# Kernel optimization log

Measured on AMD Instinct MI355X. Metric: run time of the kernel, lower is better.

## Reference

```python
import jax, jax.numpy as jnp
import numpy as np

HID = 2048      # hidden_size
EXP = 64        # moe_num_experts
TOPK = 2        # moe_top_k
TOL = 1e-4
EPS = 1e-8


def setup_inputs() -> dict:
    key = jax.random.key(0)
    kx, kw = jax.random.split(key)
    x = jax.random.normal(kx, (2048, 8, HID), dtype=jnp.float32)          # (sl, bs, hs)
    W = jax.random.normal(kw, (EXP, HID), dtype=jnp.float32) * 0.02       # router weight (E, H)
    return {"x": x, "W": W}


def sinkhorn(cost, tol=TOL):
    """Iterative Sinkhorn normalization of a (tokens, experts) cost matrix."""
    cost = jnp.exp(cost)
    n0, n1 = cost.shape

    def cond(state):
        _, _, err = state
        return err > tol

    def body(state):
        _, d1_old, _ = state
        d0 = (1.0 / n0) / (jnp.sum(d1_old * cost, axis=1) + EPS)           # (tokens,)
        d1 = (1.0 / n1) / (jnp.sum(d0[:, None] * cost, axis=0) + EPS)      # (experts,)
        err = jnp.mean(jnp.abs(d1_old - d1))
        return (d0, d1, err)

    d0 = jnp.ones((n0,), cost.dtype)
    d1 = jnp.ones((n1,), cost.dtype)
    err0 = jnp.asarray(1e9, cost.dtype)
    d0, d1, _ = jax.lax.while_loop(cond, body, (d0, d1, err0))
    return d1 * cost * d0[:, None]


def reference(x, W):
    # Training-mode path on expert-parallel rank 0 (single device reference).
    tokens = x.reshape(-1, x.shape[-1])                                    # (sl*bs, H)
    logits = tokens @ W.T                                                  # (sl*bs, E)
    # Sinkhorn assignment is computed under no_grad in the original.
    norm_logits = sinkhorn(jax.lax.stop_gradient(logits.astype(jnp.float32)))
    _, indices = jax.lax.top_k(norm_logits, TOPK)                          # (sl*bs, top_k)
    # top_k > 1 -> softmax activation (in fp32, cast back)
    probs = jax.nn.softmax(logits.astype(jnp.float32), axis=-1).astype(logits.dtype)
    scores = jnp.take_along_axis(probs, indices, axis=1)                   # (sl*bs, top_k)
    return scores, indices
```

## Files before the change

kernel.cpp:

```cpp
#include <hip/hip_runtime.h>
#include <hip/hip_cooperative_groups.h>
#include <math.h>

#define HID   2048
#define NEXP  64
#define NTOK  16384
#define SBLK  64
#define TOLF  1e-4f
#define EPSF  1e-8f

typedef _Float16 f16x8 __attribute__((ext_vector_type(8)));
typedef float    f32x4 __attribute__((ext_vector_type(4)));

__device__ __forceinline__ void cvt8(const float4 a, const float4 b,
                                     f16x8& h, f16x8& l) {
    const float v[8] = {a.x, a.y, a.z, a.w, b.x, b.y, b.z, b.w};
#pragma unroll
    for (int j = 0; j < 8; ++j) {
        const _Float16 hh = (_Float16)v[j];
        h[j] = hh;
        l[j] = (_Float16)((v[j] - (float)hh) * 2048.0f);
    }
}

#define BSTRIDE 40
#define BUFELTS (8 * 64 * BSTRIDE)

__global__ __launch_bounds__(1024, 4) void gemm_mfma(const float* __restrict__ x,
                                                     const float* __restrict__ W,
                                                     float* __restrict__ L,
                                                     int* __restrict__ cnt) {
    __shared__ __align__(16) char smem[81920];
    _Float16* Bs0 = (_Float16*)smem;
    _Float16* Bs1 = Bs0 + BUFELTS;
    float*    red = (float*)smem;

    const int tid    = (int)threadIdx.x;
    if (blockIdx.x == 0 && tid == 0) *cnt = 0;

    const int waveid = tid >> 6;
    const int wt     = waveid >> 2;
    const int wk     = waveid & 3;
    const int lane   = tid & 63;
    const int lo     = lane & 15;
    const int hi     = lane >> 4;
    const int t0     = (int)blockIdx.x * 64;
    const int kb     = wk * 512;

    const int gt    = wt * 64 + lane;
    const int srow  = gt >> 2;
    const int sfrag = gt & 3;
    const float* sgp = W + (size_t)srow * HID + kb + sfrag * 8;
    const int swh = ((wk * 2 + 0) * 64 + srow) * BSTRIDE + sfrag * 8;
    const int swl = ((wk * 2 + 1) * 64 + srow) * BSTRIDE + sfrag * 8;

    const float* xp = x + (size_t)(t0 + wt * 16 + lo) * HID + kb + hi * 8;

    f32x4 acc_hh[4], acc_hl[4];
#pragma unroll
    for (int n = 0; n < 4; ++n) {
        acc_hh[n] = f32x4{0.f, 0.f, 0.f, 0.f};
        acc_hl[n] = f32x4{0.f, 0.f, 0.f, 0.f};
    }

    {
        const float4 v0 = *(const float4*)(sgp);
        const float4 v1 = *(const float4*)(sgp + 4);
        const float4 v2 = *(const float4*)(sgp + 32);
        const float4 v3 = *(const float4*)(sgp + 36);
        f16x8 h, l;
        cvt8(v0, v1, h, l);
        *(f16x8*)&Bs0[swh] = h;
        *(f16x8*)&Bs0[swl] = l;
        cvt8(v2, v3, h, l);
        *(f16x8*)&Bs1[swh] = h;
        *(f16x8*)&Bs1[swl] = l;
    }

    float4 a0n = *(const float4*)(xp);
    float4 a1n = *(const float4*)(xp + 4);
    __syncthreads();

    float4 sv0, sv1;

#pragma unroll 2
    for (int c = 0; c < 16; ++c) {
        if (c + 2 < 16) {
            sv0 = *(const float4*)(sgp + (c + 2) * 32);
            sv1 = *(const float4*)(sgp + (c + 2) * 32 + 4);
        }

        const float4 a0 = a0n, a1 = a1n;
        const int ko = ((c + 1 < 16) ? (c + 1) : 15) * 32;
        a0n = *(const float4*)(xp + ko);
        a1n = *(const float4*)(xp + ko + 4);

        const _Float16* Bc = (c & 1) ? Bs1 : Bs0;
        f16x8 bh[4], bl[4];
#pragma unroll
        for (int n = 0; n < 4; ++n) {
            bh[n] = *(const f16x8*)&Bc[((wk * 2 + 0) * 64 + lo + n * 16) * BSTRIDE + hi * 8];
            bl[n] = *(const f16x8*)&Bc[((wk * 2 + 1) * 64 + lo + n * 16) * BSTRIDE + hi * 8];
        }

        f16x8 ah, al;
        const float av[8] = {a0.x, a0.y, a0.z, a0.w, a1.x, a1.y, a1.z, a1.w};
#pragma unroll
        for (int j = 0; j < 8; ++j) {
            const _Float16 hh = (_Float16)av[j];
            ah[j] = hh;
            al[j] = (_Float16)((av[j] - (float)hh) * 2048.0f);
        }

#pragma unroll
        for (int n = 0; n < 4; ++n)
            acc_hh[n] = __builtin_amdgcn_mfma_f32_16x16x32_f16(ah, bh[n], acc_hh[n], 0, 0, 0);
#pragma unroll
        for (int n = 0; n < 4; ++n)
            acc_hl[n] = __builtin_amdgcn_mfma_f32_16x16x32_f16(ah, bl[n], acc_hl[n], 0, 0, 0);
#pragma unroll
        for (int n = 0; n < 4; ++n)
            acc_hl[n] = __builtin_amdgcn_mfma_f32_16x16x32_f16(al, bh[n], acc_hl[n], 0, 0, 0);

        __syncthreads();

        if (c + 2 < 16) {
            _Float16* Bw = (c & 1) ? Bs1 : Bs0;
            f16x8 h, l;
            cvt8(sv0, sv1, h, l);
            *(f16x8*)&Bw[swh] = h;
            *(f16x8*)&Bw[swl] = l;
        }
    }

#pragma unroll
    for (int n = 0; n < 4; ++n)
#pragma unroll
        for (int r = 0; r < 4; ++r)
            red[waveid * 1024 + n * 256 + r * 64 + lane] =
                acc_hh[n][r] + acc_hl[n][r] * (1.0f / 2048.0f);
    __syncthreads();

    {
        const int o      = tid * 4;
        const int t_loc  = o >> 6;
        const int e      = o & 63;
        const int wt_src = t_loc >> 4;
        const int tl     = t_loc & 15;
        const int idx    = (e >> 4) * 256 + (tl & 3) * 64 + (tl >> 2) * 16 + (e & 15);
        float4 s = *(const float4*)&red[(wt_src * 4 + 0) * 1024 + idx];
#pragma unroll
        for (int q = 1; q < 4; ++q) {
            const float4 v = *(const float4*)&red[(wt_src * 4 + q) * 1024 + idx];
            s.x += v.x; s.y += v.y; s.z += v.z; s.w += v.w;
        }
        *(float4*)(L + (size_t)(t0 + t_loc) * NEXP + e) = s;
    }
}

__device__ __forceinline__ float wave_sum64(float v) {
    int x;
    float t;
    x = __builtin_bit_cast(int, v);
    t = __builtin_bit_cast(float, __builtin_amdgcn_update_dpp(0, x, 0x111, 0xf, 0xf, true)); v += t;
    x = __builtin_bit_cast(int, v);
    t = __builtin_bit_cast(float, __builtin_amdgcn_update_dpp(0, x, 0x112, 0xf, 0xf, true)); v += t;
    x = __builtin_bit_cast(int, v);
    t = __builtin_bit_cast(float, __builtin_amdgcn_update_dpp(0, x, 0x114, 0xf, 0xf, true)); v += t;
    x = __builtin_bit_cast(int, v);
    t = __builtin_bit_cast(float, __builtin_amdgcn_update_dpp(0, x, 0x118, 0xf, 0xf, true)); v += t;
    x = __builtin_bit_cast(int, v);
    t = __builtin_bit_cast(float, __builtin_amdgcn_update_dpp(0, x, 0x142, 0xa, 0xf, true)); v += t;
    x = __builtin_bit_cast(int, v);
    t = __builtin_bit_cast(float, __builtin_amdgcn_update_dpp(0, x, 0x143, 0xc, 0xf, true)); v += t;
    return __builtin_bit_cast(float, __builtin_amdgcn_readlane(__builtin_bit_cast(int, v), 63));
}

__device__ __forceinline__ void grid_barrier(int* cnt, int target) {
    __syncthreads();
    if (threadIdx.x == 0) {
        __hip_atomic_fetch_add(cnt, 1, __ATOMIC_RELEASE, __HIP_MEMORY_SCOPE_AGENT);
        int it = 0;
        for (;;) {
            int v = __hip_atomic_load(cnt, __ATOMIC_RELAXED, __HIP_MEMORY_SCOPE_AGENT);
            if (v >= target) break;
            if ((++it & 7) == 0) {
                v = __hip_atomic_load(cnt, __ATOMIC_ACQUIRE, __HIP_MEMORY_SCOPE_AGENT);
                if (v >= target) break;
            }
            __builtin_amdgcn_s_sleep(1);
        }
        (void)__hip_atomic_load(cnt, __ATOMIC_ACQUIRE, __HIP_MEMORY_SCOPE_AGENT);
    }
    __syncthreads();
}

__global__ __launch_bounds__(1024) void sinkhorn_router(const float* __restrict__ L,
                                                        float* __restrict__ colbuf,
                                                        int* __restrict__ cnt,
                                                        float* __restrict__ out,
                                                        int nh) {
    __shared__ float part[16][64];
    __shared__ float redq[64][17];
    __shared__ float d1s[64];
    __shared__ float err_s;

    const int b     = blockIdx.x;
    const int tid   = (int)threadIdx.x;
    const int w     = tid >> 6;
    const int lane  = tid & 63;
    const int tbase = b * 256 + w * 16;

    float logit[16], cost[16], dreg[16];
#pragma unroll
    for (int j = 0; j < 16; ++j) {
        const int t = tbase + j;
        float l = L[(size_t)t * NEXP + lane];
        for (int h = 1; h < nh; ++h)
            l += L[(size_t)h * NTOK * NEXP + (size_t)t * NEXP + lane];
        logit[j] = l;
        cost[j]  = expf(l);
        dreg[j]  = 0.0f;
    }

    float d1l   = 1.0f;
    float d1old = 1.0f;
    int   g     = 0;

    for (;;) {
        float colacc = 0.0f;
#pragma unroll
        for (int j = 0; j < 16; ++j) {
            const float s = wave_sum64(d1l * cost[j]);
            const float d0 = (1.0f / 16384.0f) / (s + EPSF);
            dreg[j] = d0;
            colacc = fmaf(d0, cost[j], colacc);
        }
        part[w][lane] = colacc;
        __syncthreads();

        float* cb = colbuf + (size_t)(g & 1) * (NEXP * SBLK);
        if (tid < 64) {
            float s = part[0][tid];
#pragma unroll
            for (int q = 1; q < 16; ++q) s += part[q][tid];
            cb[tid * SBLK + b] = s;
        }
        grid_barrier(cnt, 64 * (g + 1));

        {
            const int e = tid >> 4;
            const int q = tid & 15;
            const float4 v = *(const float4*)(cb + e * SBLK + q * 4);
            redq[e][q] = (v.x + v.y) + (v.z + v.w);
        }
        __syncthreads();

        if (tid < 64) {
            float tot = redq[tid][0];
#pragma unroll
            for (int q = 1; q < 16; ++q) tot += redq[tid][q];
            const float d1n = (1.0f / 64.0f) / (tot + EPSF);
            float diff = fabsf(d1old - d1n);
#pragma unroll
            for (int m = 32; m; m >>= 1) diff += __shfl_xor(diff, m, 64);
            d1s[tid] = d1n;
            d1old    = d1n;
            if (tid == 0) err_s = diff * (1.0f / 64.0f);
        }
        __syncthreads();
        d1l = d1s[lane];
        const float err = err_s;
        ++g;
        if (!(err > TOLF) || g >= 512) break;
    }

#pragma unroll 1
    for (int j = 0; j < 16; ++j) {
        const int t = tbase + j;
        const float v = (d1l * cost[j]) * dreg[j];

        float bv = v; int bi = lane;
#pragma unroll
        for (int m = 32; m; m >>= 1) {
            const float ov = __shfl_xor(bv, m, 64);
            const int   oi = __shfl_xor(bi, m, 64);
            if (ov > bv || (ov == bv && oi < bi)) { bv = ov; bi = oi; }
        }
        const int i1 = bi;

        const float v2 = (lane == i1) ? -INFINITY : v;
        float bv2 = v2; int bi2 = lane;
#pragma unroll
        for (int m = 32; m; m >>= 1) {
            const float ov = __shfl_xor(bv2, m, 64);
            const int   oi = __shfl_xor(bi2, m, 64);
            if (ov > bv2 || (ov == bv2 && oi < bi2)) { bv2 = ov; bi2 = oi; }
        }
        const int i2 = bi2;

        float mx = logit[j];
#pragma unroll
        for (int m = 32; m; m >>= 1) mx = fmaxf(mx, __shfl_xor(mx, m, 64));
        const float e = expf(logit[j] - mx);
        float se = e;
#pragma unroll
        for (int m = 32; m; m >>= 1) se += __shfl_xor(se, m, 64);

        const float p1 = __shfl(e, i1, 64) / se;
        const float p2 = __shfl(e, i2, 64) / se;

        if (lane == 0) {
            out[(size_t)t * 2 + 0] = p1;
            out[(size_t)t * 2 + 1] = p2;
            out[(size_t)NTOK * 2 + (size_t)t * 2 + 0] = (float)i1;
            out[(size_t)NTOK * 2 + (size_t)t * 2 + 1] = (float)i2;
        }
    }
}

extern "C" void kernel_launch(void* const* d_in, const int* in_sizes, int n_in,
                              void* d_out, int out_size, void* d_ws, size_t ws_size,
                              hipStream_t stream) {
    const float* x = (const float*)d_in[0];
    const float* W = (const float*)d_in[1];
    float* out = (float*)d_out;

    float* L      = (float*)d_ws;
    float* colbuf = L + (size_t)NTOK * NEXP;
    int*   cnt    = (int*)(colbuf + 2 * NEXP * SBLK);

    gemm_mfma<<<dim3(256), dim3(1024), 0, stream>>>(x, W, L, cnt);

    int nh = 1;
    void* args[] = { (void*)&L, (void*)&colbuf, (void*)&cnt, (void*)&out, (void*)&nh };
    hipLaunchCooperativeKernel((void*)sinkhorn_router, dim3(SBLK), dim3(1024),
                               args, 0, stream);
}
```

Baseline: 274.8 us.

## Use hierarchical tree grid barrier and deepen GEMM prefetch pipeline

The flat single-counter grid barrier in the Sinkhorn kernel becomes a two-level tree: 8 padded leaf counters, a root counter and a generation flag that waiters poll. This spreads atomic contention across several cache lines. Separately, the GEMM loop now prefetches x two chunks ahead and W three chunks ahead, issuing those loads after the compute to hide global latency. The cost is more live registers, and the counter buffer must hold 320 ints, all zeroed by the first GEMM block.

```diff
diff --git a/kernel.cpp b/kernel.cpp
--- a/kernel.cpp
+++ b/kernel.cpp
@@ -25,6 +25,7 @@
 
 #define BSTRIDE 40
 #define BUFELTS (8 * 64 * BSTRIDE)
+#define LEAFSTRIDE 32
 
 __global__ __launch_bounds__(1024, 4) void gemm_mfma(const float* __restrict__ x,
                                                      const float* __restrict__ W,
@@ -35,8 +36,8 @@
     _Float16* Bs1 = Bs0 + BUFELTS;
     float*    red = (float*)smem;
 
-    const int tid    = (int)threadIdx.x;
-    if (blockIdx.x == 0 && tid == 0) *cnt = 0;
+    const int tid = (int)threadIdx.x;
+    if (blockIdx.x == 0 && tid < 10 * LEAFSTRIDE) cnt[tid] = 0;
 
     const int waveid = tid >> 6;
     const int wt     = waveid >> 2;
@@ -63,38 +64,29 @@
         acc_hl[n] = f32x4{0.f, 0.f, 0.f, 0.f};
     }
 
+    float4 sv0 = *(const float4*)(sgp);
+    float4 sv1 = *(const float4*)(sgp + 4);
     {
-        const float4 v0 = *(const float4*)(sgp);
-        const float4 v1 = *(const float4*)(sgp + 4);
-        const float4 v2 = *(const float4*)(sgp + 32);
-        const float4 v3 = *(const float4*)(sgp + 36);
+        const float4 t2 = *(const float4*)(sgp + 32);
+        const float4 t3 = *(const float4*)(sgp + 36);
         f16x8 h, l;
-        cvt8(v0, v1, h, l);
+        cvt8(sv0, sv1, h, l);
         *(f16x8*)&Bs0[swh] = h;
         *(f16x8*)&Bs0[swl] = l;
-        cvt8(v2, v3, h, l);
+        cvt8(t2, t3, h, l);
         *(f16x8*)&Bs1[swh] = h;
         *(f16x8*)&Bs1[swl] = l;
     }
-
-    float4 a0n = *(const float4*)(xp);
-    float4 a1n = *(const float4*)(xp + 4);
+    float4 a0c = *(const float4*)(xp);
+    float4 a1c = *(const float4*)(xp + 4);
+    float4 a0n = *(const float4*)(xp + 32);
+    float4 a1n = *(const float4*)(xp + 36);
+    sv0 = *(const float4*)(sgp + 64);
+    sv1 = *(const float4*)(sgp + 68);
     __syncthreads();
-
-    float4 sv0, sv1;
 
 #pragma unroll 2
     for (int c = 0; c < 16; ++c) {
-        if (c + 2 < 16) {
-            sv0 = *(const float4*)(sgp + (c + 2) * 32);
-            sv1 = *(const float4*)(sgp + (c + 2) * 32 + 4);
-        }
-
-        const float4 a0 = a0n, a1 = a1n;
-        const int ko = ((c + 1 < 16) ? (c + 1) : 15) * 32;
-        a0n = *(const float4*)(xp + ko);
-        a1n = *(const float4*)(xp + ko + 4);
-
         const _Float16* Bc = (c & 1) ? Bs1 : Bs0;
         f16x8 bh[4], bl[4];
 #pragma unroll
@@ -104,7 +96,7 @@
         }
 
         f16x8 ah, al;
-        const float av[8] = {a0.x, a0.y, a0.z, a0.w, a1.x, a1.y, a1.z, a1.w};
+        const float av[8] = {a0c.x, a0c.y, a0c.z, a0c.w, a1c.x, a1c.y, a1c.z, a1c.w};
 #pragma unroll
         for (int j = 0; j < 8; ++j) {
             const _Float16 hh = (_Float16)av[j];
@@ -130,6 +122,15 @@
             cvt8(sv0, sv1, h, l);
             *(f16x8*)&Bw[swh] = h;
             *(f16x8*)&Bw[swl] = l;
+        }
+        a0c = a0n; a1c = a1n;
+        if (c + 2 < 16) {
+            a0n = *(const float4*)(xp + (c + 2) * 32);
+            a1n = *(const float4*)(xp + (c + 2) * 32 + 4);
+        }
+        if (c + 3 < 16) {
+            sv0 = *(const float4*)(sgp + (c + 3) * 32);
+            sv1 = *(const float4*)(sgp + (c + 3) * 32 + 4);
         }
     }
 
@@ -176,21 +177,29 @@
     return __builtin_bit_cast(float, __builtin_amdgcn_readlane(__builtin_bit_cast(int, v), 63));
 }
 
-__device__ __forceinline__ void grid_barrier(int* cnt, int target) {
+__device__ __forceinline__ void grid_barrier(int* cnt, int g) {
     __syncthreads();
     if (threadIdx.x == 0) {
-        __hip_atomic_fetch_add(cnt, 1, __ATOMIC_RELEASE, __HIP_MEMORY_SCOPE_AGENT);
+        int* leaf = cnt + ((int)blockIdx.x & 7) * LEAFSTRIDE;
+        int* root = cnt + 8 * LEAFSTRIDE;
+        int* gen  = cnt + 9 * LEAFSTRIDE;
+        const int old = __hip_atomic_fetch_add(leaf, 1, __ATOMIC_ACQ_REL, __HIP_MEMORY_SCOPE_AGENT);
+        if ((old & 7) == 7) {
+            const int r = __hip_atomic_fetch_add(root, 1, __ATOMIC_ACQ_REL, __HIP_MEMORY_SCOPE_AGENT);
+            if ((r & 7) == 7)
+                __hip_atomic_store(gen, g + 1, __ATOMIC_RELEASE, __HIP_MEMORY_SCOPE_AGENT);
+        }
         int it = 0;
         for (;;) {
-            int v = __hip_atomic_load(cnt, __ATOMIC_RELAXED, __HIP_MEMORY_SCOPE_AGENT);
-            if (v >= target) break;
+            int v = __hip_atomic_load(gen, __ATOMIC_RELAXED, __HIP_MEMORY_SCOPE_AGENT);
+            if (v >= g + 1) break;
             if ((++it & 7) == 0) {
-                v = __hip_atomic_load(cnt, __ATOMIC_ACQUIRE, __HIP_MEMORY_SCOPE_AGENT);
-                if (v >= target) break;
+                v = __hip_atomic_load(gen, __ATOMIC_ACQUIRE, __HIP_MEMORY_SCOPE_AGENT);
+                if (v >= g + 1) break;
             }
             __builtin_amdgcn_s_sleep(1);
         }
-        (void)__hip_atomic_load(cnt, __ATOMIC_ACQUIRE, __HIP_MEMORY_SCOPE_AGENT);
+        (void)__hip_atomic_load(gen, __ATOMIC_ACQUIRE, __HIP_MEMORY_SCOPE_AGENT);
     }
     __syncthreads();
 }
@@ -246,7 +255,7 @@
             for (int q = 1; q < 16; ++q) s += part[q][tid];
             cb[tid * SBLK + b] = s;
         }
-        grid_barrier(cnt, 64 * (g + 1));
+        grid_barrier(cnt, g);
 
         {
             const int e = tid >> 4;
```

After: 271.7 us. Within noise of the previous version (-1.1%).
